# Kernel optimization log

Hardware: AMD Instinct MI355X
Metric: run time of the kernel (lower is better)

The kernel has to match this reference:

```python
import jax, jax.numpy as jnp
import numpy as np

NUM_EXPERT = 64
TOP_K = 2
N_TOKENS = 16384
H_DIM = 4096


def setup_inputs() -> dict:
    key = jax.random.key(0)
    k1, k2, k3 = jax.random.split(key, 3)
    x = jax.random.normal(k1, (N_TOKENS, H_DIM), dtype=jnp.float32)
    # nn.Linear(h_dim, num_expert): weight [E, H], bias [E]
    W = jax.random.normal(k2, (NUM_EXPERT, H_DIM), dtype=jnp.float32) * (1.0 / np.sqrt(H_DIM))
    b = jax.random.normal(k3, (NUM_EXPERT,), dtype=jnp.float32) * 0.01
    return {"x": x, "W": W, "b": b}


def reference(x, W, b):
    # gating linear: [N, H] @ [H, E] + [E] -> [N, E]
    router_logits = x @ W.T + b
    # softmax over experts in float32 (matches dtype=torch.float)
    router_probs = jax.nn.softmax(router_logits.astype(jnp.float32), axis=1)
    # top-k over experts (values sorted descending, like torch.topk)
    router_weights, selected_experts_idx = jax.lax.top_k(router_probs, TOP_K)
    # renormalize via second softmax over the top_k dim (dim=1 of [N, K])
    router_weights = jax.nn.softmax(router_weights, axis=1).astype(x.dtype)
    # one-hot expert mask [N, K, E] -> permute(2,1,0) -> [E, K, N]
    expert_mask = jax.nn.one_hot(selected_experts_idx, NUM_EXPERT, dtype=jnp.int32)
    expert_mask = jnp.transpose(expert_mask, (2, 1, 0))
    return router_logits, router_weights, selected_experts_idx, expert_mask
```

## Files before the change

kernel.cpp:

```cpp
#include <hip/hip_runtime.h>
#include <hip/hip_bf16.h>
#include <math.h>

#define H_DIM 4096
#define N_EXP 64
#define N_TOK 16384
#define BM    32
#define KB    64
#define NCHUNK (H_DIM / KB)
#define MARGIN 1e-3f
#define SLOT_BYTES 24576

typedef __attribute__((ext_vector_type(8))) short short8v;
typedef __attribute__((ext_vector_type(4))) short short4v;
typedef __attribute__((ext_vector_type(4))) float float4v;

__device__ __forceinline__ unsigned short bf16_rn(float f) {
    unsigned u = __builtin_bit_cast(unsigned, f);
    u += 0x7FFFu + ((u >> 16) & 1u);
    return (unsigned short)(u >> 16);
}
__device__ __forceinline__ float bf16_hi_f32(unsigned u) {
    return __builtin_bit_cast(float, u & 0xFFFF0000u);
}
__device__ __forceinline__ void gload_lds16(const void* g, void* l) {
    __builtin_amdgcn_global_load_lds(
        (const __attribute__((address_space(1))) unsigned int*)g,
        (__attribute__((address_space(3))) unsigned int*)l, 16, 0, 0);
}

__global__ __launch_bounds__(256)
void wconvert_kernel(const float* __restrict__ W,
                     unsigned short* __restrict__ wh,
                     unsigned short* __restrict__ wm,
                     int* __restrict__ counter) {
    int i = blockIdx.x * 256 + threadIdx.x;
    if (i == 0) *counter = 0;
    float4 w = ((const float4*)W)[i];
    float f[4] = {w.x, w.y, w.z, w.w};
    short4v hv, mv;
#pragma unroll
    for (int j = 0; j < 4; ++j) {
        unsigned u = __builtin_bit_cast(unsigned, f[j]);
        hv[j] = (short)(u >> 16);
        mv[j] = (short)bf16_rn(f[j] - bf16_hi_f32(u));
    }
    ((short4v*)wh)[i] = hv;
    ((short4v*)wm)[i] = mv;
}

__global__ __launch_bounds__(512, 4)
void router_mfma_kernel(const float* __restrict__ x,
                        const unsigned short* __restrict__ wh,
                        const unsigned short* __restrict__ wm,
                        const float* __restrict__ bias,
                        float* __restrict__ logits,
                        float* __restrict__ wout,
                        float* __restrict__ iout,
                        int* __restrict__ counter,
                        int* __restrict__ list) {
    __shared__ char smem[2 * SLOT_BYTES];
    float* olds = (float*)smem;

    const int tid  = threadIdx.x;
    const int lane = tid & 63;
    const int wid  = __builtin_amdgcn_readfirstlane(tid >> 6);
    const int tok0 = blockIdx.x * BM;

    const int q    = lane >> 4;
    const int e15  = lane & 15;
    const int mt   = wid & 1;
    const int eg   = wid >> 1;
    const int arow = mt * 16 + e15;
    const int er   = eg * 16 + e15;

    float4v acc = {0.f, 0.f, 0.f, 0.f};

    auto stage = [&](int slot, int kc) {
        char* base = smem + slot * SLOT_BYTES;
        {
            int row = tid >> 4, u = tid & 15;
            int us  = u ^ (row & 15);
            const float* src = x + (size_t)(tok0 + row) * H_DIM + kc + us * 4;
            gload_lds16(src, base + (size_t)(wid * 64) * 16);
        }
#pragma unroll
        for (int j = 0; j < 2; ++j) {
            int idx = j * 512 + tid;
            int s = idx >> 9, e = (idx >> 3) & 63, u = idx & 7;
            int us = u ^ (e & 7);
            const unsigned short* wsrc = s ? wm : wh;
            const unsigned short* src  = wsrc + (size_t)e * H_DIM + kc + us * 8;
            gload_lds16(src, base + 8192 + (size_t)(j * 512 + wid * 64) * 16);
        }
    };

    auto compute = [&](int slot) {
        const char* xc = smem + slot * SLOT_BYTES;
        const char* wc = xc + 8192;
#pragma unroll
        for (int t = 0; t < 2; ++t) {
            float f[8];
#pragma unroll
            for (int h = 0; h < 2; ++h) {
                int u = (t * 8 + q * 2 + h) ^ (arow & 15);
                float4 a = *(const float4*)(xc + (size_t)(arow * 16 + u) * 16);
                f[h * 4 + 0] = a.x; f[h * 4 + 1] = a.y;
                f[h * 4 + 2] = a.z; f[h * 4 + 3] = a.w;
            }
            short8v ah, am;
#pragma unroll
            for (int j = 0; j < 8; ++j) {
                unsigned u = __builtin_bit_cast(unsigned, f[j]);
                ah[j] = (short)(u >> 16);
                am[j] = (short)bf16_rn(f[j] - bf16_hi_f32(u));
            }
            int up = (t * 4 + q) ^ (e15 & 7);
            short8v bh = *(const short8v*)(wc + (size_t)(er * 8 + up) * 16);
            short8v bm = *(const short8v*)(wc + 8192 + (size_t)(er * 8 + up) * 16);

            acc = __builtin_amdgcn_mfma_f32_16x16x32_bf16(ah, bh, acc, 0, 0, 0);
            acc = __builtin_amdgcn_mfma_f32_16x16x32_bf16(am, bh, acc, 0, 0, 0);
            acc = __builtin_amdgcn_mfma_f32_16x16x32_bf16(ah, bm, acc, 0, 0, 0);
            acc = __builtin_amdgcn_mfma_f32_16x16x32_bf16(am, bm, acc, 0, 0, 0);
        }
    };

    stage(0, 0);
    for (int c = 0; c < NCHUNK; ++c) {
        __builtin_amdgcn_s_barrier();
        if (c + 1 < NCHUNK) {
            stage((c + 1) & 1, (c + 1) * KB);
            asm volatile("s_waitcnt vmcnt(3)" ::: "memory");
        } else {
            asm volatile("s_waitcnt vmcnt(0)" ::: "memory");
        }
        __builtin_amdgcn_s_barrier();
        compute(c & 1);
    }
    __syncthreads();

    float bv = bias[er];
#pragma unroll
    for (int r = 0; r < 4; ++r) {
        int trow = mt * 16 + q * 4 + r;
        float v = acc[r] + bv;
        logits[(size_t)(tok0 + trow) * N_EXP + er] = v;
        olds[trow * 66 + er] = v;
    }
    __syncthreads();

#pragma unroll
    for (int it = 0; it < 4; ++it) {
        const int nl = wid * 4 + it;
        const int n  = tok0 + nl;
        float l = olds[nl * 66 + lane];

        float v1 = l; int i1 = lane;
#pragma unroll
        for (int off = 32; off >= 1; off >>= 1) {
            float ov = __shfl_xor(v1, off);
            int   oi = __shfl_xor(i1, off);
            if (ov > v1 || (ov == v1 && oi < i1)) { v1 = ov; i1 = oi; }
        }
        float l2 = (lane == i1) ? -INFINITY : l;
        float v2 = l2; int i2 = lane;
#pragma unroll
        for (int off = 32; off >= 1; off >>= 1) {
            float ov = __shfl_xor(v2, off);
            int   oi = __shfl_xor(i2, off);
            if (ov > v2 || (ov == v2 && oi < i2)) { v2 = ov; i2 = oi; }
        }
        float l3 = (lane == i1 || lane == i2) ? -INFINITY : l;
        float v3 = l3;
#pragma unroll
        for (int off = 32; off >= 1; off >>= 1)
            v3 = fmaxf(v3, __shfl_xor(v3, off));

        float Z = expf(l - v1);
#pragma unroll
        for (int off = 32; off >= 1; off >>= 1) Z += __shfl_xor(Z, off);

        if (lane == 0) {
            float p1 = 1.0f / Z;
            float p2 = expf(v2 - v1) / Z;
            float t  = expf(p2 - p1);
            wout[2 * n + 0] = 1.0f / (1.0f + t);
            wout[2 * n + 1] = t / (1.0f + t);
            iout[2 * n + 0] = (float)i1;
            iout[2 * n + 1] = (float)i2;
            if ((v1 - v2 < MARGIN) || (v2 - v3 < MARGIN)) {
                int sidx = atomicAdd(counter, 1);
                list[sidx] = n;
            }
        }
    }
}

__global__ __launch_bounds__(256)
void router_logits_f32(const float* __restrict__ x,
                       const float* __restrict__ W,
                       const float* __restrict__ bias,
                       float* __restrict__ logits) {
    __shared__ float4 wlds[32 * 64];
    __shared__ float4 xlds[32][32];
    const int tid = threadIdx.x;
    const int lane = tid & 63;
    const int wid = __builtin_amdgcn_readfirstlane(tid >> 6);
    const int tok0b = blockIdx.x * 32;
    const int trow0 = wid * 8;
    float acc[8];
#pragma unroll
    for (int t = 0; t < 8; ++t) acc[t] = 0.0f;
    for (int kc = 0; kc < H_DIM; kc += 128) {
        __syncthreads();
#pragma unroll
        for (int i = 0; i < 8; ++i) {
            int idx = tid + i * 256;
            int se = idx >> 5, sj = idx & 31;
            float4 v = *(const float4*)(W + (size_t)se * H_DIM + kc + sj * 4);
            wlds[sj * 64 + (se ^ (sj & 7))] = v;
        }
#pragma unroll
        for (int i = 0; i < 4; ++i) {
            int idx = tid + i * 256;
            int row = idx >> 5, col = idx & 31;
            xlds[row][col] = *(const float4*)(x + (size_t)(tok0b + row) * H_DIM + kc + col * 4);
        }
        __syncthreads();
#pragma unroll 4
        for (int jg = 0; jg < 32; ++jg) {
            float4 w = wlds[jg * 64 + (lane ^ (jg & 7))];
#pragma unroll
            for (int t = 0; t < 8; ++t) {
                float4 xv = xlds[trow0 + t][jg];
                acc[t] = fmaf(w.x, xv.x, acc[t]);
                acc[t] = fmaf(w.y, xv.y, acc[t]);
                acc[t] = fmaf(w.z, xv.z, acc[t]);
                acc[t] = fmaf(w.w, xv.w, acc[t]);
            }
        }
    }
    float bv = bias[lane];
#pragma unroll
    for (int t = 0; t < 8; ++t)
        logits[(size_t)(tok0b + trow0 + t) * N_EXP + lane] = acc[t] + bv;
}

__global__ __launch_bounds__(256)
void topk_kernel(const float* __restrict__ logits,
                 float* __restrict__ wout,
                 float* __restrict__ iout) {
    const int lane = threadIdx.x & 63;
    const int wid  = threadIdx.x >> 6;
    const int wg   = blockIdx.x * 4 + wid;
#pragma unroll
    for (int it = 0; it < 4; ++it) {
        const int n = wg * 4 + it;
        float l = logits[(size_t)n * N_EXP + lane];
        float v1 = l; int i1 = lane;
#pragma unroll
        for (int off = 32; off >= 1; off >>= 1) {
            float ov = __shfl_xor(v1, off);
            int   oi = __shfl_xor(i1, off);
            if (ov > v1 || (ov == v1 && oi < i1)) { v1 = ov; i1 = oi; }
        }
        float l2 = (lane == i1) ? -INFINITY : l;
        float v2 = l2; int i2 = lane;
#pragma unroll
        for (int off = 32; off >= 1; off >>= 1) {
            float ov = __shfl_xor(v2, off);
            int   oi = __shfl_xor(i2, off);
            if (ov > v2 || (ov == v2 && oi < i2)) { v2 = ov; i2 = oi; }
        }
        float Z = expf(l - v1);
#pragma unroll
        for (int off = 32; off >= 1; off >>= 1) Z += __shfl_xor(Z, off);
        if (lane == 0) {
            float p1 = 1.0f / Z;
            float p2 = expf(v2 - v1) / Z;
            float t  = expf(p2 - p1);
            wout[2 * n + 0] = 1.0f / (1.0f + t);
            wout[2 * n + 1] = t / (1.0f + t);
            iout[2 * n + 0] = (float)i1;
            iout[2 * n + 1] = (float)i2;
        }
    }
}

__global__ __launch_bounds__(256)
void fixup_kernel(const float* __restrict__ x,
                  const float* __restrict__ W,
                  const float* __restrict__ bias,
                  float* __restrict__ wout,
                  float* __restrict__ iout,
                  const int* __restrict__ counter,
                  const int* __restrict__ list) {
    __shared__ float plds[4][64];
    __shared__ float llds[64];
    int cnt = counter[0];
    if (cnt > N_TOK) cnt = N_TOK;
    const int e = threadIdx.x & 63;
    const int s = threadIdx.x >> 6;
    for (int it = blockIdx.x; it < cnt; it += 128) {
        int n = list[it];
        const float4* xr = (const float4*)(x + (size_t)n * H_DIM) + s * 256;
        const float4* wr = (const float4*)(W + (size_t)e * H_DIM) + s * 256;
        float p = 0.f;
#pragma unroll 8
        for (int j = 0; j < 256; ++j) {
            float4 a = xr[j], w = wr[j];
            p = fmaf(a.x, w.x, p); p = fmaf(a.y, w.y, p);
            p = fmaf(a.z, w.z, p); p = fmaf(a.w, w.w, p);
        }
        plds[s][e] = p;
        __syncthreads();
        if (threadIdx.x < 64)
            llds[e] = ((plds[0][e] + plds[1][e]) + (plds[2][e] + plds[3][e])) + bias[e];
        __syncthreads();
        if (threadIdx.x == 0) {
            float v1 = -INFINITY, v2 = -INFINITY;
            int i1 = 0, i2 = 0;
            for (int i = 0; i < 64; ++i) {
                float li = llds[i];
                if (li > v1)      { v2 = v1; i2 = i1; v1 = li; i1 = i; }
                else if (li > v2) { v2 = li; i2 = i; }
            }
            float Z = 0.0f;
            for (int i = 0; i < 64; ++i) Z += expf(llds[i] - v1);
            float p1 = 1.0f / Z;
            float p2 = expf(v2 - v1) / Z;
            float t  = expf(p2 - p1);
            wout[2 * n + 0] = 1.0f / (1.0f + t);
            wout[2 * n + 1] = t / (1.0f + t);
            iout[2 * n + 0] = (float)i1;
            iout[2 * n + 1] = (float)i2;
        }
        __syncthreads();
    }
}

__global__ __launch_bounds__(256)
void mask_kernel(const float* __restrict__ iout,
                 float* __restrict__ mask) {
    int g4  = blockIdx.x * 256 + threadIdx.x;
    int gid = g4 * 4;
    int n0  = gid & (N_TOK - 1);
    int ek  = gid >> 14;
    float ef = (float)(ek >> 1);
    int  ko  = ek & 1;
    float4 v;
    v.x = (iout[(size_t)(n0 + 0) * 2 + ko] == ef) ? 1.0f : 0.0f;
    v.y = (iout[(size_t)(n0 + 1) * 2 + ko] == ef) ? 1.0f : 0.0f;
    v.z = (iout[(size_t)(n0 + 2) * 2 + ko] == ef) ? 1.0f : 0.0f;
    v.w = (iout[(size_t)(n0 + 3) * 2 + ko] == ef) ? 1.0f : 0.0f;
    ((float4*)mask)[g4] = v;
}

extern "C" void kernel_launch(void* const* d_in, const int* in_sizes, int n_in,
                              void* d_out, int out_size, void* d_ws, size_t ws_size,
                              hipStream_t stream) {
    const float* x  = (const float*)d_in[0];
    const float* W  = (const float*)d_in[1];
    const float* b  = (const float*)d_in[2];

    float* out    = (float*)d_out;
    float* logits = out;
    float* wout   = logits + (size_t)N_TOK * 64;
    float* iout   = wout   + (size_t)N_TOK * 2;
    float* mask   = iout   + (size_t)N_TOK * 2;

    const size_t wsplit = (size_t)N_EXP * H_DIM;
    const size_t need   = 2 * wsplit * sizeof(unsigned short) + 4 + (size_t)N_TOK * 4;
    if (ws_size >= need) {
        unsigned short* wh = (unsigned short*)d_ws;
        unsigned short* wm = wh + wsplit;
        int* counter = (int*)((char*)d_ws + 2 * wsplit * sizeof(unsigned short));
        int* list    = counter + 1;
        wconvert_kernel<<<(int)(wsplit / 4 / 256), 256, 0, stream>>>(W, wh, wm, counter);
        router_mfma_kernel<<<N_TOK / BM, 512, 0, stream>>>(x, wh, wm, b, logits,
                                                           wout, iout, counter, list);
        fixup_kernel<<<128, 256, 0, stream>>>(x, W, b, wout, iout, counter, list);
    } else {
        router_logits_f32<<<N_TOK / 32, 256, 0, stream>>>(x, W, b, logits);
        topk_kernel<<<N_TOK / 16, 256, 0, stream>>>(logits, wout, iout);
    }
    mask_kernel<<<(N_EXP * 2 * N_TOK) / 4 / 256, 256, 0, stream>>>(iout, mask);
}
```

Measured before the change: 150.2 us.

## Split K across waves with per-wave W staging and direct x register loads

Blocks now cover 16 tokens with 4 waves instead of 32 tokens with 8 waves. Each wave handles a 1024-wide K slice for all 64 experts, keeping four accumulators. Each wave loads its x fragments straight from global into registers and double-buffers its own W chunks in private LDS, so the block-wide barriers in the K loop go away. A cross-wave LDS reduction at the end adds the partial sums and the bias. The cost is that every block still streams the full split W while covering half as many tokens, which doubles W traffic from L2, and each iteration waits on vmcnt(0), which limits overlap of loads with compute.

```diff
diff --git a/kernel.cpp b/kernel.cpp
--- a/kernel.cpp
+++ b/kernel.cpp
@@ -5,11 +5,13 @@
 #define H_DIM 4096
 #define N_EXP 64
 #define N_TOK 16384
-#define BM    32
-#define KB    64
-#define NCHUNK (H_DIM / KB)
+#define BM    16
+#define KSL   1024
+#define CH    32
+#define NCH   (KSL / CH)
+#define WSLOT 8192
+#define WREG  16384
 #define MARGIN 1e-3f
-#define SLOT_BYTES 24576
 
 typedef __attribute__((ext_vector_type(8))) short short8v;
 typedef __attribute__((ext_vector_type(4))) short short4v;
@@ -49,7 +51,7 @@
     ((short4v*)wm)[i] = mv;
 }
 
-__global__ __launch_bounds__(512, 4)
+__global__ __launch_bounds__(256, 2)
 void router_mfma_kernel(const float* __restrict__ x,
                         const unsigned short* __restrict__ wh,
                         const unsigned short* __restrict__ wm,
@@ -59,94 +61,100 @@
                         float* __restrict__ iout,
                         int* __restrict__ counter,
                         int* __restrict__ list) {
-    __shared__ char smem[2 * SLOT_BYTES];
-    float* olds = (float*)smem;
+    __shared__ char smem[4 * WREG];
 
     const int tid  = threadIdx.x;
     const int lane = tid & 63;
     const int wid  = __builtin_amdgcn_readfirstlane(tid >> 6);
     const int tok0 = blockIdx.x * BM;
 
-    const int q    = lane >> 4;
-    const int e15  = lane & 15;
-    const int mt   = wid & 1;
-    const int eg   = wid >> 1;
-    const int arow = mt * 16 + e15;
-    const int er   = eg * 16 + e15;
-
-    float4v acc = {0.f, 0.f, 0.f, 0.f};
-
-    auto stage = [&](int slot, int kc) {
-        char* base = smem + slot * SLOT_BYTES;
-        {
-            int row = tid >> 4, u = tid & 15;
-            int us  = u ^ (row & 15);
-            const float* src = x + (size_t)(tok0 + row) * H_DIM + kc + us * 4;
-            gload_lds16(src, base + (size_t)(wid * 64) * 16);
-        }
-#pragma unroll
-        for (int j = 0; j < 2; ++j) {
-            int idx = j * 512 + tid;
-            int s = idx >> 9, e = (idx >> 3) & 63, u = idx & 7;
-            int us = u ^ (e & 7);
-            const unsigned short* wsrc = s ? wm : wh;
-            const unsigned short* src  = wsrc + (size_t)e * H_DIM + kc + us * 8;
-            gload_lds16(src, base + 8192 + (size_t)(j * 512 + wid * 64) * 16);
+    const int q     = lane >> 4;
+    const int e15   = lane & 15;
+    const int kbase = wid * KSL;
+    const int uq    = q ^ ((e15 >> 1) & 3);
+
+    char* const wreg = smem + wid * WREG;
+
+    const float* xp = x + (size_t)(tok0 + e15) * H_DIM + kbase + q * 8;
+
+    float4v acc0 = {0.f,0.f,0.f,0.f}, acc1 = {0.f,0.f,0.f,0.f};
+    float4v acc2 = {0.f,0.f,0.f,0.f}, acc3 = {0.f,0.f,0.f,0.f};
+
+    auto stageW = [&](char* slotbase, int k0) {
+#pragma unroll
+        for (int j = 0; j < 8; ++j) {
+            int unit = j * 64 + lane;
+            int t = unit >> 8;
+            int e = (unit >> 2) & 63;
+            int u = unit & 3;
+            int us = u ^ ((e >> 1) & 3);
+            const unsigned short* src =
+                (t ? wm : wh) + (size_t)e * H_DIM + k0 + us * 8;
+            gload_lds16(src, slotbase + j * 1024);
         }
     };
 
-    auto compute = [&](int slot) {
-        const char* xc = smem + slot * SLOT_BYTES;
-        const char* wc = xc + 8192;
-#pragma unroll
-        for (int t = 0; t < 2; ++t) {
-            float f[8];
-#pragma unroll
-            for (int h = 0; h < 2; ++h) {
-                int u = (t * 8 + q * 2 + h) ^ (arow & 15);
-                float4 a = *(const float4*)(xc + (size_t)(arow * 16 + u) * 16);
-                f[h * 4 + 0] = a.x; f[h * 4 + 1] = a.y;
-                f[h * 4 + 2] = a.z; f[h * 4 + 3] = a.w;
-            }
-            short8v ah, am;
-#pragma unroll
-            for (int j = 0; j < 8; ++j) {
-                unsigned u = __builtin_bit_cast(unsigned, f[j]);
-                ah[j] = (short)(u >> 16);
-                am[j] = (short)bf16_rn(f[j] - bf16_hi_f32(u));
-            }
-            int up = (t * 4 + q) ^ (e15 & 7);
-            short8v bh = *(const short8v*)(wc + (size_t)(er * 8 + up) * 16);
-            short8v bm = *(const short8v*)(wc + 8192 + (size_t)(er * 8 + up) * 16);
-
-            acc = __builtin_amdgcn_mfma_f32_16x16x32_bf16(ah, bh, acc, 0, 0, 0);
-            acc = __builtin_amdgcn_mfma_f32_16x16x32_bf16(am, bh, acc, 0, 0, 0);
-            acc = __builtin_amdgcn_mfma_f32_16x16x32_bf16(ah, bm, acc, 0, 0, 0);
-            acc = __builtin_amdgcn_mfma_f32_16x16x32_bf16(am, bm, acc, 0, 0, 0);
-        }
+    auto computeC = [&](const char* slotbase, float4 a0, float4 a1) {
+        float f[8] = {a0.x,a0.y,a0.z,a0.w,a1.x,a1.y,a1.z,a1.w};
+        short8v ah, am;
+#pragma unroll
+        for (int j = 0; j < 8; ++j) {
+            unsigned u = __builtin_bit_cast(unsigned, f[j]);
+            ah[j] = (short)(u >> 16);
+            am[j] = (short)bf16_rn(f[j] - bf16_hi_f32(u));
+        }
+#define GSTEP(g, ACC)                                                          \
+        {   const char* p = slotbase + (size_t)(((g) * 16 + e15) * 4 + uq) * 16; \
+            short8v bh = *(const short8v*)(p);                                 \
+            short8v bm = *(const short8v*)(p + 4096);                          \
+            ACC = __builtin_amdgcn_mfma_f32_16x16x32_bf16(ah, bh, ACC, 0, 0, 0); \
+            ACC = __builtin_amdgcn_mfma_f32_16x16x32_bf16(am, bh, ACC, 0, 0, 0); \
+            ACC = __builtin_amdgcn_mfma_f32_16x16x32_bf16(ah, bm, ACC, 0, 0, 0); \
+            ACC = __builtin_amdgcn_mfma_f32_16x16x32_bf16(am, bm, ACC, 0, 0, 0); }
+        GSTEP(0, acc0)
+        GSTEP(1, acc1)
+        GSTEP(2, acc2)
+        GSTEP(3, acc3)
+#undef GSTEP
     };
 
-    stage(0, 0);
-    for (int c = 0; c < NCHUNK; ++c) {
-        __builtin_amdgcn_s_barrier();
-        if (c + 1 < NCHUNK) {
-            stage((c + 1) & 1, (c + 1) * KB);
-            asm volatile("s_waitcnt vmcnt(3)" ::: "memory");
-        } else {
-            asm volatile("s_waitcnt vmcnt(0)" ::: "memory");
-        }
-        __builtin_amdgcn_s_barrier();
-        compute(c & 1);
+    stageW(wreg, kbase);
+    asm volatile("s_waitcnt vmcnt(0)" ::: "memory");
+
+    for (int s = 0; s < NCH; ++s) {
+        char* cur = wreg + (s & 1) * WSLOT;
+        if (s + 1 < NCH)
+            stageW(wreg + ((s + 1) & 1) * WSLOT, kbase + (s + 1) * CH);
+        float4 a0 = *(const float4*)(xp + (size_t)s * CH);
+        float4 a1 = *(const float4*)(xp + (size_t)s * CH + 4);
+        computeC(cur, a0, a1);
+        asm volatile("s_waitcnt vmcnt(0)" ::: "memory");
+    }
+
+    {
+        float* part = (float*)wreg;
+#pragma unroll
+        for (int r = 0; r < 4; ++r) {
+            int trow = q * 4 + r;
+            part[trow * 66 +  0 + e15] = acc0[r];
+            part[trow * 66 + 16 + e15] = acc1[r];
+            part[trow * 66 + 32 + e15] = acc2[r];
+            part[trow * 66 + 48 + e15] = acc3[r];
+        }
     }
     __syncthreads();
 
-    float bv = bias[er];
-#pragma unroll
-    for (int r = 0; r < 4; ++r) {
-        int trow = mt * 16 + q * 4 + r;
-        float v = acc[r] + bv;
-        logits[(size_t)(tok0 + trow) * N_EXP + er] = v;
-        olds[trow * 66 + er] = v;
+    float* olds = (float*)(smem + 3 * WREG + WSLOT);
+#pragma unroll
+    for (int i = 0; i < 4; ++i) {
+        int o  = i * 256 + tid;
+        int tk = o >> 6, e = o & 63;
+        float v = bias[e];
+#pragma unroll
+        for (int w = 0; w < 4; ++w)
+            v += ((const float*)(smem + w * WREG))[tk * 66 + e];
+        logits[(size_t)(tok0 + tk) * N_EXP + e] = v;
+        olds[tk * 66 + e] = v;
     }
     __syncthreads();
 
@@ -378,7 +386,7 @@
         int* counter = (int*)((char*)d_ws + 2 * wsplit * sizeof(unsigned short));
         int* list    = counter + 1;
         wconvert_kernel<<<(int)(wsplit / 4 / 256), 256, 0, stream>>>(W, wh, wm, counter);
-        router_mfma_kernel<<<N_TOK / BM, 512, 0, stream>>>(x, wh, wm, b, logits,
+        router_mfma_kernel<<<N_TOK / BM, 256, 0, stream>>>(x, wh, wm, b, logits,
                                                            wout, iout, counter, list);
         fixup_kernel<<<128, 256, 0, stream>>>(x, W, b, wout, iout, counter, list);
     } else {
```

After: 201.3 us. 1.34x slower.
